# Kernel optimization log

Hardware: AMD Instinct MI355X
Metric: run time of the kernel (lower is better)

Reference implementation:

```python
import jax, jax.numpy as jnp
import numpy as np

WEIGHT = 1.0  # config['weight']


def setup_inputs() -> dict:
    key = jax.random.key(0)
    ks = jax.random.split(key, 10)
    B, N, S, C, D, E, H, V = 8, 4096, 512, 16, 1024, 256, 1024, 100000
    return {
        "span_vecs": jax.random.normal(ks[0], (B, N, D), jnp.float32),
        "ent_table": jax.random.normal(ks[1], (V, E), jnp.float32) * 0.02,
        "W1": jax.random.normal(ks[2], (D + E, H), jnp.float32) * (1.0 / np.sqrt(D + E)),
        "b1": jnp.zeros((H,), jnp.float32),
        "W2": jax.random.normal(ks[3], (H,), jnp.float32) * (1.0 / np.sqrt(H)),
        "b2": jnp.zeros((), jnp.float32),
        "targets_all": jax.random.uniform(ks[4], (B, N, C), jnp.float32),
        "linker_indices": jax.random.randint(ks[5], (B, S), 0, N, jnp.int32),
        "candidates_all": jax.random.randint(ks[6], (B, N, C), 0, V, jnp.int32),
        "candidate_lengths_all": jax.random.randint(ks[7], (B, N), 0, C + 1, jnp.int32),
    }


def reference(span_vecs, ent_table, W1, b1, W2, b2, targets_all,
              linker_indices, candidates_all, candidate_lengths_all):
    D = span_vecs.shape[-1]
    C = candidates_all.shape[-1]
    idx = linker_indices  # [B, S]

    # batched_index_select gathers over the span axis
    candidates = jnp.take_along_axis(candidates_all, idx[:, :, None], axis=1)        # [B,S,C] int
    lengths = jnp.take_along_axis(candidate_lengths_all, idx, axis=1)                # [B,S] int
    targets = jnp.take_along_axis(targets_all, idx[:, :, None], axis=1)              # [B,S,C]
    linker_vecs = jnp.take_along_axis(span_vecs, idx[:, :, None], axis=1)            # [B,S,D]

    cand_vecs = ent_table[candidates]                                                # [B,S,C,E]

    # layers: Linear(D+E,H) -> ReLU -> (dropout=identity in eval) -> Linear(H,1)
    # fused: split W1 so the [B,S,C,D+E] expanded concat is never materialized
    W1s, W1e = W1[:D], W1[D:]
    h_span = jnp.einsum('bsd,dh->bsh', linker_vecs, W1s)                             # [B,S,H]
    h_cand = jnp.einsum('bsce,eh->bsch', cand_vecs, W1e)                             # [B,S,C,H]
    h = jax.nn.relu(h_span[:, :, None, :] + h_cand + b1)
    scores = jnp.einsum('bsch,h->bsc', h, W2) + b2                                   # [B,S,C]

    # create_candidate_mask
    mask = (jnp.arange(C)[None, None, :] < lengths[:, :, None]).astype(scores.dtype)

    # BCEWithLogitsLoss(reduction='none'), masked sum * weight
    bce = jnp.maximum(scores, 0.0) - scores * targets + jnp.log1p(jnp.exp(-jnp.abs(scores)))
    loss = (mask * bce).sum() * WEIGHT

    predictions = jnp.argmax(scores - (1.0 - mask) * 1e23, axis=-1)                  # [B,S]
    return loss, scores, predictions
```

## Files before the change

### kernel.cpp

```cpp
#include <hip/hip_runtime.h>
#include <math.h>


typedef short short8 __attribute__((ext_vector_type(8)));
typedef _Float16 half8v __attribute__((ext_vector_type(8)));
typedef float f32x16 __attribute__((ext_vector_type(16)));

static __device__ inline unsigned short f2bf(float x) {
  unsigned u = __float_as_uint(x);
  unsigned r = (u + 0x7FFFu + ((u >> 16) & 1u)) >> 16;
  return (unsigned short)r;
}
static __device__ inline float bf2f(unsigned short b) {
  return __uint_as_float(((unsigned)b) << 16);
}
static __device__ inline unsigned short f2h(float x) {
  _Float16 h = (_Float16)x;
  return *(unsigned short*)&h;
}

#define GLD_TO_LDS(gp, lp)                                          \
  __builtin_amdgcn_global_load_lds(                                 \
      (const __attribute__((address_space(1))) void*)(gp),          \
      (__attribute__((address_space(3))) void*)(lp), 16, 0, 0)

static __device__ inline void split_write(unsigned short* buf, int g,
                                          float4 c0, float4 c1) {
  float xs[8] = {c0.x, c0.y, c0.z, c0.w, c1.x, c1.y, c1.z, c1.w};
  short8 h8, l8;
#pragma unroll
  for (int j = 0; j < 8; ++j) {
    unsigned short h = f2bf(xs[j]);
    h8[j] = (short)h;
    l8[j] = (short)f2bf(xs[j] - bf2f(h));
  }
  *(short8*)(buf + (g << 3)) = h8;
  *(short8*)(buf + 4096 + (g << 3)) = l8;
}

static __device__ inline void h16_write(unsigned short* buf, int g,
                                        float4 c0, float4 c1) {
  short8 v;
  v[0] = (short)f2h(c0.x); v[1] = (short)f2h(c0.y);
  v[2] = (short)f2h(c0.z); v[3] = (short)f2h(c0.w);
  v[4] = (short)f2h(c1.x); v[5] = (short)f2h(c1.y);
  v[6] = (short)f2h(c1.z); v[7] = (short)f2h(c1.w);
  *(short8*)(buf + (g << 3)) = v;
}

__global__ __launch_bounds__(256) void k_w1t(const float* __restrict__ W1,
                                             unsigned short* __restrict__ sThi,
                                             unsigned short* __restrict__ sTlo,
                                             unsigned short* __restrict__ eT16) {
  __shared__ float t[32][33];
  int n0 = blockIdx.x * 32, k0 = blockIdx.y * 32;
  int rr = threadIdx.x >> 5, cc = threadIdx.x & 31;
#pragma unroll
  for (int i = 0; i < 4; ++i)
    t[rr + 8 * i][cc] = W1[(size_t)(k0 + rr + 8 * i) * 1024 + n0 + cc];
  __syncthreads();
#pragma unroll
  for (int i = 0; i < 4; ++i) {
    int nl = rr + 8 * i;
    float v = t[cc][nl];
    int n = n0 + nl, k = k0 + cc;
    if (k0 < 1024) {
      unsigned short h = f2bf(v);
      unsigned short l = f2bf(v - bf2f(h));
      sThi[(size_t)n * 1024 + k] = h;
      sTlo[(size_t)n * 1024 + k] = l;
    } else {
      eT16[(size_t)n * 256 + (k - 1024)] = f2h(v);
    }
  }
}

template <int KSTEPS>
__global__ __launch_bounds__(256, 2) void k_g32g(
    const float* __restrict__ span, const int* __restrict__ linker,
    const unsigned short* __restrict__ Bhi, const unsigned short* __restrict__ Blo,
    float* __restrict__ Out) {
  const int tid = threadIdx.x;
  const int l = tid & 63;
  const int w = tid >> 6;
  const int wm = w >> 1, wn = w & 1;
  const int id = blockIdx.x;
  const int z = id >> 8;
  const int sid = id & 255;
  const int m8 = sid & 7;
  const int cb = (sid >> 3) & 7;
  const int q = sid >> 6;
  const int row0 = ((q << 3) + m8) << 7;
  const int col0 = cb << 7;
  const int koff = z * (KSTEPS * 32);
  Out += (size_t)z * 4194304;

  __shared__ unsigned short lds[32768];

  f32x16 acc[2][2];
#pragma unroll
  for (int i = 0; i < 2; ++i)
#pragma unroll
    for (int j = 0; j < 2; ++j)
#pragma unroll
      for (int k = 0; k < 16; ++k) acc[i][j][k] = 0.f;

  const int ar0 = tid >> 2, ap0 = tid & 3;
  const int al0c = ap0 ^ ((ar0 >> 1) & 3);
  const int ar1 = ar0 + 64;
  const int al1c = ap0 ^ ((ar1 >> 1) & 3);
  const int r0g = row0 + ar0, r1g = row0 + ar1;
  const float* asrc0 =
      span + (((size_t)(r0g >> 9) << 12) + linker[r0g]) * 1024 + koff + al0c * 8;
  const float* asrc1 =
      span + (((size_t)(r1g >> 9) << 12) + linker[r1g]) * 1024 + koff + al1c * 8;
  const size_t boff0 = (size_t)(col0 + ar0) * 1024 + al0c * 8 + koff;
  const size_t boff1 = (size_t)(col0 + ar1) * 1024 + al1c * 8 + koff;
  const int w512 = w * 512;

  {
    float4 a00 = *(const float4*)(asrc0);
    float4 a01 = *(const float4*)(asrc0 + 4);
    float4 a10 = *(const float4*)(asrc1);
    float4 a11 = *(const float4*)(asrc1 + 4);
    GLD_TO_LDS(Bhi + boff0, lds + 8192 + w512);
    GLD_TO_LDS(Bhi + boff1, lds + 10240 + w512);
    GLD_TO_LDS(Blo + boff0, lds + 12288 + w512);
    GLD_TO_LDS(Blo + boff1, lds + 14336 + w512);
    split_write(lds, tid, a00, a01);
    split_write(lds, tid + 256, a10, a11);
  }
  asm volatile("s_waitcnt vmcnt(0) lgkmcnt(0)" ::: "memory");
  __builtin_amdgcn_s_barrier();
  asm volatile("" ::: "memory");

  for (int ks = 0; ks < KSTEPS; ++ks) {
    float4 a00, a01, a10, a11;
    const int k0n = (ks + 1) * 32;
    unsigned short* bn = lds + (((ks + 1) & 1) << 14);
    if (ks + 1 < KSTEPS) {
      a00 = *(const float4*)(asrc0 + k0n);
      a01 = *(const float4*)(asrc0 + k0n + 4);
      a10 = *(const float4*)(asrc1 + k0n);
      a11 = *(const float4*)(asrc1 + k0n + 4);
      GLD_TO_LDS(Bhi + boff0 + k0n, bn + 8192 + w512);
      GLD_TO_LDS(Bhi + boff1 + k0n, bn + 10240 + w512);
      GLD_TO_LDS(Blo + boff0 + k0n, bn + 12288 + w512);
      GLD_TO_LDS(Blo + boff1 + k0n, bn + 14336 + w512);
    }

    const unsigned short* cbuf = lds + ((ks & 1) << 14);
#pragma unroll
    for (int kc = 0; kc < 2; ++kc) {
      const int kg = kc * 2 + (l >> 5);
      short8 ah[2], alv[2], bh[2], bl[2];
#pragma unroll
      for (int it = 0; it < 2; ++it) {
        int r = wm * 64 + it * 32 + (l & 31);
        int off = r * 32 + ((kg ^ ((r >> 1) & 3)) << 3);
        ah[it] = *(const short8*)(cbuf + off);
        alv[it] = *(const short8*)(cbuf + 4096 + off);
      }
#pragma unroll
      for (int jt = 0; jt < 2; ++jt) {
        int r = wn * 64 + jt * 32 + (l & 31);
        int off = r * 32 + ((kg ^ ((r >> 1) & 3)) << 3);
        bh[jt] = *(const short8*)(cbuf + 8192 + off);
        bl[jt] = *(const short8*)(cbuf + 12288 + off);
      }
#pragma unroll
      for (int it = 0; it < 2; ++it)
#pragma unroll
        for (int jt = 0; jt < 2; ++jt) {
          acc[it][jt] = __builtin_amdgcn_mfma_f32_32x32x16_bf16(
              ah[it], bh[jt], acc[it][jt], 0, 0, 0);
          acc[it][jt] = __builtin_amdgcn_mfma_f32_32x32x16_bf16(
              ah[it], bl[jt], acc[it][jt], 0, 0, 0);
          acc[it][jt] = __builtin_amdgcn_mfma_f32_32x32x16_bf16(
              alv[it], bh[jt], acc[it][jt], 0, 0, 0);
        }
    }

    if (ks + 1 < KSTEPS) {
      split_write(bn, tid, a00, a01);
      split_write(bn, tid + 256, a10, a11);
      asm volatile("s_waitcnt vmcnt(0) lgkmcnt(0)" ::: "memory");
      __builtin_amdgcn_s_barrier();
      asm volatile("" ::: "memory");
    }
  }

#pragma unroll
  for (int it = 0; it < 2; ++it) {
    int mb = row0 + wm * 64 + it * 32 + 4 * (l >> 5);
#pragma unroll
    for (int jt = 0; jt < 2; ++jt) {
      int n = col0 + wn * 64 + jt * 32 + (l & 31);
#pragma unroll
      for (int rg = 0; rg < 16; ++rg) {
        int m = mb + (rg & 3) + 8 * (rg >> 2);
        Out[(size_t)m * 1024 + n] = acc[it][jt][rg];
      }
    }
  }
}

__global__ __launch_bounds__(256, 4) void k_gf16g(
    const float* __restrict__ ent, const int* __restrict__ linker,
    const int* __restrict__ cand_all, const unsigned short* __restrict__ Bt,
    const float* __restrict__ HsIn, const float* __restrict__ b1,
    const float* __restrict__ W2, float* __restrict__ Out) {
  const int tid = threadIdx.x;
  const int l = tid & 63;
  const int w = tid >> 6;
  const int wm = w >> 1, wn = w & 1;
  const int id = blockIdx.x;
  const int m8 = id & 7;
  const int cb = (id >> 3) & 7;
  const int q = id >> 6;
  const int row0 = ((q << 3) + m8) << 7;
  const int col0 = cb << 7;

  __shared__ unsigned short lds[16384];

  f32x16 acc[2][2];
#pragma unroll
  for (int i = 0; i < 2; ++i)
#pragma unroll
    for (int j = 0; j < 2; ++j)
#pragma unroll
      for (int k = 0; k < 16; ++k) acc[i][j][k] = 0.f;

  const int ar0 = tid >> 2, ap0 = tid & 3;
  const int al0c = ap0 ^ ((ar0 >> 1) & 3);
  const int ar1 = ar0 + 64;
  const int al1c = ap0 ^ ((ar1 >> 1) & 3);
  const int s0 = row0 + ar0, s1 = row0 + ar1;
  const int cid0 =
      cand_all[(((size_t)(s0 >> 13) << 12) + linker[s0 >> 4]) * 16 + (s0 & 15)];
  const int cid1 =
      cand_all[(((size_t)(s1 >> 13) << 12) + linker[s1 >> 4]) * 16 + (s1 & 15)];
  const float* asrc0 = ent + ((size_t)cid0 << 8) + al0c * 8;
  const float* asrc1 = ent + ((size_t)cid1 << 8) + al1c * 8;
  const size_t boff0 = (size_t)(col0 + ar0) * 256 + al0c * 8;
  const size_t boff1 = (size_t)(col0 + ar1) * 256 + al1c * 8;
  const int w512 = w * 512;

  {
    float4 a00 = *(const float4*)(asrc0);
    float4 a01 = *(const float4*)(asrc0 + 4);
    float4 a10 = *(const float4*)(asrc1);
    float4 a11 = *(const float4*)(asrc1 + 4);
    GLD_TO_LDS(Bt + boff0, lds + 4096 + w512);
    GLD_TO_LDS(Bt + boff1, lds + 6144 + w512);
    h16_write(lds, tid, a00, a01);
    h16_write(lds, tid + 256, a10, a11);
  }
  asm volatile("s_waitcnt vmcnt(0) lgkmcnt(0)" ::: "memory");
  __builtin_amdgcn_s_barrier();
  asm volatile("" ::: "memory");

#pragma unroll 2
  for (int ks = 0; ks < 8; ++ks) {
    float4 a00, a01, a10, a11;
    const int k0n = (ks + 1) * 32;
    unsigned short* bn = lds + (((ks + 1) & 1) << 13);
    if (ks + 1 < 8) {
      a00 = *(const float4*)(asrc0 + k0n);
      a01 = *(const float4*)(asrc0 + k0n + 4);
      a10 = *(const float4*)(asrc1 + k0n);
      a11 = *(const float4*)(asrc1 + k0n + 4);
      GLD_TO_LDS(Bt + boff0 + k0n, bn + 4096 + w512);
      GLD_TO_LDS(Bt + boff1 + k0n, bn + 6144 + w512);
    }

    const unsigned short* cbuf = lds + ((ks & 1) << 13);
#pragma unroll
    for (int kc = 0; kc < 2; ++kc) {
      const int kg = kc * 2 + (l >> 5);
      half8v av[2], bv[2];
#pragma unroll
      for (int it = 0; it < 2; ++it) {
        int r = wm * 64 + it * 32 + (l & 31);
        int off = r * 32 + ((kg ^ ((r >> 1) & 3)) << 3);
        av[it] = *(const half8v*)(cbuf + off);
      }
#pragma unroll
      for (int jt = 0; jt < 2; ++jt) {
        int r = wn * 64 + jt * 32 + (l & 31);
        int off = r * 32 + ((kg ^ ((r >> 1) & 3)) << 3);
        bv[jt] = *(const half8v*)(cbuf + 4096 + off);
      }
#pragma unroll
      for (int it = 0; it < 2; ++it)
#pragma unroll
        for (int jt = 0; jt < 2; ++jt)
          acc[it][jt] = __builtin_amdgcn_mfma_f32_32x32x16_f16(
              av[it], bv[jt], acc[it][jt], 0, 0, 0);
    }

    if (ks + 1 < 8) {
      h16_write(bn, tid, a00, a01);
      h16_write(bn, tid + 256, a10, a11);
      asm volatile("s_waitcnt vmcnt(0) lgkmcnt(0)" ::: "memory");
      __builtin_amdgcn_s_barrier();
      asm volatile("" ::: "memory");
    }
  }

  float sv[2][16];
#pragma unroll
  for (int it = 0; it < 2; ++it) {
#pragma unroll
    for (int rg = 0; rg < 16; ++rg) sv[it][rg] = 0.f;
    const int p0 = (row0 + wm * 64 + it * 32) >> 4;
#pragma unroll
    for (int jt = 0; jt < 2; ++jt) {
      int n = col0 + wn * 64 + jt * 32 + (l & 31);
      float b1v = b1[n], w2v = W2[n];
      float add0 = HsIn[(size_t)p0 * 1024 + n] +
                   HsIn[4194304 + (size_t)p0 * 1024 + n] + b1v;
      float add1 = HsIn[(size_t)(p0 + 1) * 1024 + n] +
                   HsIn[4194304 + (size_t)(p0 + 1) * 1024 + n] + b1v;
#pragma unroll
      for (int rg = 0; rg < 16; ++rg) {
        float h = fmaxf(acc[it][jt][rg] + (rg < 8 ? add0 : add1), 0.f);
        sv[it][rg] = fmaf(h, w2v, sv[it][rg]);
      }
    }
  }
  __syncthreads();
  float* scf = (float*)lds;
  const int cc0 = l & 31, lh4 = 4 * (l >> 5);
#pragma unroll
  for (int it = 0; it < 2; ++it)
#pragma unroll
    for (int rg = 0; rg < 16; ++rg) {
      int row = (rg & 3) + 8 * (rg >> 2) + lh4;
      scf[((w * 2 + it) * 32 + row) * 32 + ((cc0 + row) & 31)] = sv[it][rg];
    }
  __syncthreads();
  int gr = tid >> 1, h = tid & 1;
  int r = gr & 31, itv = (gr >> 5) & 1, wmv = gr >> 6;
  const float* sa = scf + ((wmv * 4 + itv) * 32 + r) * 32;
  const float* sb = scf + ((wmv * 4 + 2 + itv) * 32 + r) * 32;
  float sum = 0.f;
#pragma unroll
  for (int j = 0; j < 16; ++j) {
    int cidx = (h * 16 + j + r) & 31;
    sum += sa[cidx] + sb[cidx];
  }
  sum += __shfl_xor(sum, 1, 64);
  if (h == 0) Out[(size_t)cb * 65536 + row0 + gr] = sum;
}

__global__ __launch_bounds__(64) void k_final8(const float* __restrict__ score8,
                                               const float* __restrict__ b2p,
                                               const float* __restrict__ targets_all,
                                               const int* __restrict__ linker,
                                               const int* __restrict__ len_all,
                                               float* __restrict__ out) {
  int p = blockIdx.x * 64 + threadIdx.x;
  float b2 = b2p[0];
  int b = p >> 9;
  int i = linker[p];
  int len = len_all[(b << 12) + i];
  const float* tg = targets_all + ((((size_t)b << 12) + (size_t)i) << 4);

  float sc[16];
#pragma unroll
  for (int c = 0; c < 16; ++c) sc[c] = b2;
#pragma unroll
  for (int c8 = 0; c8 < 8; ++c8) {
    const float4* q4 = (const float4*)(score8 + (size_t)c8 * 65536 + p * 16);
#pragma unroll
    for (int j = 0; j < 4; ++j) {
      float4 v = q4[j];
      sc[j * 4 + 0] += v.x; sc[j * 4 + 1] += v.y;
      sc[j * 4 + 2] += v.z; sc[j * 4 + 3] += v.w;
    }
  }

  float loss = 0.f;
  float best = -INFINITY;
  int bc = 0;
#pragma unroll
  for (int c = 0; c < 16; ++c) {
    float s = sc[c];
    out[1 + p * 16 + c] = s;
    float val;
    if (c < len) {
      float t = tg[c];
      loss += fmaxf(s, 0.f) - s * t + log1pf(expf(-fabsf(s)));
      val = s;
    } else {
      val = s - 1e23f;
    }
    if (val > best) { best = val; bc = c; }
  }
  out[1 + 65536 + p] = (float)bc;

  for (int off = 32; off > 0; off >>= 1) loss += __shfl_down(loss, off, 64);
  if (threadIdx.x == 0) atomicAdd(out, loss);
}

#define BM 128
#define BN 128
#define BK 16
#define PAD 4

__global__ __launch_bounds__(256) void k_prep(const int* __restrict__ linker,
                                              const int* __restrict__ cand_all,
                                              int* __restrict__ cand_ids) {
  int g = blockIdx.x * 256 + threadIdx.x;
  int pair = g >> 4;
  int c = g & 15;
  int b = pair >> 9;
  int i = linker[pair];
  cand_ids[g] = cand_all[(((size_t)b << 12) + (size_t)i) * 16 + c];
}

__global__ __launch_bounds__(256) void k_hs(const float* __restrict__ span,
                                            const float* __restrict__ W1,
                                            const int* __restrict__ linker,
                                            float* __restrict__ Hs) {
  const int tid = threadIdx.x;
  const int tx = tid & 15, ty = tid >> 4;
  const int row0 = blockIdx.y * BM;
  const int col0 = blockIdx.x * BN;
  __shared__ float As[BK][BM + PAD];
  __shared__ float Bs[BK][BN + PAD];
  __shared__ int rows_g[BM];
  if (tid < BM) {
    int m = row0 + tid;
    int b = m >> 9;
    rows_g[tid] = (b << 12) + linker[m];
  }
  __syncthreads();
  float acc[8][8] = {};
  for (int k0 = 0; k0 < 1024; k0 += BK) {
#pragma unroll
    for (int ll = 0; ll < 2; ++ll) {
      int f = tid + ll * 256;
      int r = f >> 2;
      int kk = (f & 3) << 2;
      const float4 v = *(const float4*)(span + (size_t)rows_g[r] * 1024 + k0 + kk);
      As[kk + 0][r] = v.x; As[kk + 1][r] = v.y;
      As[kk + 2][r] = v.z; As[kk + 3][r] = v.w;
    }
#pragma unroll
    for (int ll = 0; ll < 2; ++ll) {
      int f = tid + ll * 256;
      int kk = f >> 5;
      int nn = (f & 31) << 2;
      *(float4*)&Bs[kk][nn] = *(const float4*)(W1 + (size_t)(k0 + kk) * 1024 + col0 + nn);
    }
    __syncthreads();
#pragma unroll
    for (int k = 0; k < BK; ++k) {
      float a[8], b[8];
      *(float4*)&a[0] = *(const float4*)&As[k][ty * 8];
      *(float4*)&a[4] = *(const float4*)&As[k][ty * 8 + 4];
      *(float4*)&b[0] = *(const float4*)&Bs[k][tx * 8];
      *(float4*)&b[4] = *(const float4*)&Bs[k][tx * 8 + 4];
#pragma unroll
      for (int i = 0; i < 8; ++i)
#pragma unroll
        for (int j = 0; j < 8; ++j) acc[i][j] = fmaf(a[i], b[j], acc[i][j]);
    }
    __syncthreads();
  }
#pragma unroll
  for (int i = 0; i < 8; ++i) {
    int m = row0 + ty * 8 + i;
    float* dst = Hs + (size_t)m * 1024 + col0 + tx * 8;
    *(float4*)dst = *(float4*)&acc[i][0];
    *(float4*)(dst + 4) = *(float4*)&acc[i][4];
  }
}

__global__ __launch_bounds__(256) void k_hc(const float* __restrict__ ent,
                                            const float* __restrict__ W1,
                                            const int* __restrict__ cand_ids,
                                            const float* __restrict__ Hs,
                                            const float* __restrict__ b1,
                                            const float* __restrict__ W2,
                                            float* __restrict__ score_ws) {
  const int tid = threadIdx.x;
  const int tx = tid & 15, ty = tid >> 4;
  const int row0 = blockIdx.y * BM;
  const int col0 = blockIdx.x * BN;
  __shared__ float As[BK][BM + PAD];
  __shared__ float Bs[BK][BN + PAD];
  __shared__ int rows_g[BM];
  __shared__ float red[BM][17];
  if (tid < BM) rows_g[tid] = cand_ids[row0 + tid];
  __syncthreads();
  float acc[8][8] = {};
  for (int k0 = 0; k0 < 256; k0 += BK) {
#pragma unroll
    for (int ll = 0; ll < 2; ++ll) {
      int f = tid + ll * 256;
      int r = f >> 2;
      int kk = (f & 3) << 2;
      const float4 v = *(const float4*)(ent + (size_t)rows_g[r] * 256 + k0 + kk);
      As[kk + 0][r] = v.x; As[kk + 1][r] = v.y;
      As[kk + 2][r] = v.z; As[kk + 3][r] = v.w;
    }
#pragma unroll
    for (int ll = 0; ll < 2; ++ll) {
      int f = tid + ll * 256;
      int kk = f >> 5;
      int nn = (f & 31) << 2;
      *(float4*)&Bs[kk][nn] =
          *(const float4*)(W1 + (size_t)(1024 + k0 + kk) * 1024 + col0 + nn);
    }
    __syncthreads();
#pragma unroll
    for (int k = 0; k < BK; ++k) {
      float a[8], b[8];
      *(float4*)&a[0] = *(const float4*)&As[k][ty * 8];
      *(float4*)&a[4] = *(const float4*)&As[k][ty * 8 + 4];
      *(float4*)&b[0] = *(const float4*)&Bs[k][tx * 8];
      *(float4*)&b[4] = *(const float4*)&Bs[k][tx * 8 + 4];
#pragma unroll
      for (int i = 0; i < 8; ++i)
#pragma unroll
        for (int j = 0; j < 8; ++j) acc[i][j] = fmaf(a[i], b[j], acc[i][j]);
    }
    __syncthreads();
  }
  const int pair = (row0 + ty * 8) >> 4;
  float hsv[8], b1v[8], w2v[8];
  {
    const float* hp = Hs + (size_t)pair * 1024 + col0 + tx * 8;
    *(float4*)&hsv[0] = *(const float4*)hp;
    *(float4*)&hsv[4] = *(const float4*)(hp + 4);
    const float* bp = b1 + col0 + tx * 8;
    *(float4*)&b1v[0] = *(const float4*)bp;
    *(float4*)&b1v[4] = *(const float4*)(bp + 4);
    const float* wp = W2 + col0 + tx * 8;
    *(float4*)&w2v[0] = *(const float4*)wp;
    *(float4*)&w2v[4] = *(const float4*)(wp + 4);
  }
#pragma unroll
  for (int i = 0; i < 8; ++i) {
    float s = 0.f;
#pragma unroll
    for (int j = 0; j < 8; ++j) {
      float h = acc[i][j] + hsv[j] + b1v[j];
      h = fmaxf(h, 0.f);
      s = fmaf(h, w2v[j], s);
    }
    red[ty * 8 + i][tx] = s;
  }
  __syncthreads();
  if (tid < BM) {
    float s = 0.f;
#pragma unroll
    for (int x = 0; x < 16; ++x) s += red[tid][x];
    atomicAdd(&score_ws[row0 + tid], s);
  }
}

__global__ __launch_bounds__(256) void k_final(const float* __restrict__ score_ws,
                                               const float* __restrict__ b2p,
                                               const float* __restrict__ targets_all,
                                               const int* __restrict__ linker,
                                               const int* __restrict__ len_all,
                                               float* __restrict__ out) {
  int p = blockIdx.x * 256 + threadIdx.x;
  float b2 = b2p[0];
  int b = p >> 9;
  int i = linker[p];
  int len = len_all[(b << 12) + i];
  const float* tg = targets_all + ((((size_t)b << 12) + (size_t)i) << 4);

  float loss = 0.f;
  float best = -INFINITY;
  int bc = 0;
#pragma unroll
  for (int c = 0; c < 16; ++c) {
    float sc = score_ws[p * 16 + c] + b2;
    out[1 + p * 16 + c] = sc;
    float val;
    if (c < len) {
      float t = tg[c];
      loss += fmaxf(sc, 0.f) - sc * t + log1pf(expf(-fabsf(sc)));
      val = sc;
    } else {
      val = sc - 1e23f;
    }
    if (val > best) { best = val; bc = c; }
  }
  out[1 + 65536 + p] = (float)bc;

  for (int off = 32; off > 0; off >>= 1) loss += __shfl_down(loss, off, 64);
  if ((threadIdx.x & 63) == 0) atomicAdd(out, loss);
}

extern "C" void kernel_launch(void* const* d_in, const int* in_sizes, int n_in,
                              void* d_out, int out_size, void* d_ws,
                              size_t ws_size, hipStream_t stream) {
  const float* span    = (const float*)d_in[0];
  const float* ent     = (const float*)d_in[1];
  const float* W1      = (const float*)d_in[2];
  const float* b1      = (const float*)d_in[3];
  const float* W2      = (const float*)d_in[4];
  const float* b2      = (const float*)d_in[5];
  const float* targets = (const float*)d_in[6];
  const int* linker    = (const int*)d_in[7];
  const int* cand_all  = (const int*)d_in[8];
  const int* len_all   = (const int*)d_in[9];
  float* out = (float*)d_out;

  char* ws = (char*)d_ws;
  float* Hs       = (float*)(ws + 0);
  float* score8   = (float*)(ws + 33554432);
  unsigned short* sTh  = (unsigned short*)(ws + 35651584);
  unsigned short* sTl  = (unsigned short*)(ws + 37748736);
  unsigned short* eT16 = (unsigned short*)(ws + 39845888);
  float* score_ws = (float*)(ws + 40370176);
  int* cand_ids   = (int*)(ws + 40632320);
  const size_t NEED_MFMA = 40894464;

  hipMemsetAsync(d_out, 0, sizeof(float), stream);

  if (ws_size >= NEED_MFMA) {
    k_w1t<<<dim3(32, 40), dim3(256), 0, stream>>>(W1, sTh, sTl, eT16);
    k_g32g<16><<<dim3(512), dim3(256), 0, stream>>>(span, linker, sTh, sTl, Hs);
    k_gf16g<<<dim3(4096), dim3(256), 0, stream>>>(ent, linker, cand_all, eT16,
                                                  Hs, b1, W2, score8);
    k_final8<<<dim3(64), dim3(64), 0, stream>>>(score8, b2, targets, linker,
                                                len_all, out);
  } else {
    hipMemsetAsync(score_ws, 0, 65536 * sizeof(float), stream);
    k_prep<<<dim3(256), dim3(256), 0, stream>>>(linker, cand_all, cand_ids);
    dim3 g1(8, 32);
    k_hs<<<g1, dim3(256), 0, stream>>>(span, W1, linker, Hs);
    dim3 g2(8, 512);
    k_hc<<<g2, dim3(256), 0, stream>>>(ent, W1, cand_ids, Hs, b1, W2, score_ws);
    k_final<<<dim3(16), dim3(256), 0, stream>>>(score_ws, b2, targets, linker,
                                                len_all, out);
  }
}
```

Measured before the change: 339.3 us.

## Pre-gather candidate embeddings to fp16 buffer and stream via direct LDS loads

Adds a prep phase, merged into the W1 transpose kernel, that gathers the candidate entity rows, converts them to fp16 and writes them into a contiguous workspace buffer. The main candidate GEMM then loads A tiles with global_load_lds like B, dropping the per-iteration fp32 register loads and conversions. The cost is an extra 32MB fp16 write and read-back pass and a larger workspace requirement, traded for a simpler, better pipelined GEMM inner loop.

```diff
diff --git a/kernel.cpp b/kernel.cpp
--- a/kernel.cpp
+++ b/kernel.cpp
@@ -38,39 +38,44 @@
   *(short8*)(buf + 4096 + (g << 3)) = l8;
 }
 
-static __device__ inline void h16_write(unsigned short* buf, int g,
-                                        float4 c0, float4 c1) {
-  short8 v;
-  v[0] = (short)f2h(c0.x); v[1] = (short)f2h(c0.y);
-  v[2] = (short)f2h(c0.z); v[3] = (short)f2h(c0.w);
-  v[4] = (short)f2h(c1.x); v[5] = (short)f2h(c1.y);
-  v[6] = (short)f2h(c1.z); v[7] = (short)f2h(c1.w);
-  *(short8*)(buf + (g << 3)) = v;
-}
-
-__global__ __launch_bounds__(256) void k_w1t(const float* __restrict__ W1,
-                                             unsigned short* __restrict__ sThi,
-                                             unsigned short* __restrict__ sTlo,
-                                             unsigned short* __restrict__ eT16) {
+__global__ __launch_bounds__(256) void k_prep_e(
+    const float* __restrict__ ent, const float* __restrict__ W1,
+    const int* __restrict__ linker, const int* __restrict__ cand_all,
+    unsigned short* __restrict__ A2, unsigned short* __restrict__ sThi,
+    unsigned short* __restrict__ sTlo, unsigned short* __restrict__ eT16) {
   __shared__ float t[32][33];
-  int n0 = blockIdx.x * 32, k0 = blockIdx.y * 32;
-  int rr = threadIdx.x >> 5, cc = threadIdx.x & 31;
-#pragma unroll
-  for (int i = 0; i < 4; ++i)
-    t[rr + 8 * i][cc] = W1[(size_t)(k0 + rr + 8 * i) * 1024 + n0 + cc];
-  __syncthreads();
-#pragma unroll
-  for (int i = 0; i < 4; ++i) {
-    int nl = rr + 8 * i;
-    float v = t[cc][nl];
-    int n = n0 + nl, k = k0 + cc;
-    if (k0 < 1024) {
-      unsigned short h = f2bf(v);
-      unsigned short l = f2bf(v - bf2f(h));
-      sThi[(size_t)n * 1024 + k] = h;
-      sTlo[(size_t)n * 1024 + k] = l;
-    } else {
-      eT16[(size_t)n * 256 + (k - 1024)] = f2h(v);
+  const int bx = blockIdx.x;
+  if (bx < 16384) {
+    int f = bx * 256 + threadIdx.x;
+    int row = f >> 6;
+    int pair = row >> 4;
+    int b = pair >> 9;
+    int i = linker[pair];
+    int cid = cand_all[(((size_t)b << 12) + (size_t)i) * 16 + (row & 15)];
+    const float4 v = *((const float4*)(ent + ((size_t)cid << 8)) + (f & 63));
+    *(ushort4*)(A2 + ((size_t)f << 2)) =
+        make_ushort4(f2h(v.x), f2h(v.y), f2h(v.z), f2h(v.w));
+  } else {
+    int b2x = bx - 16384;
+    int n0 = (b2x & 31) * 32, k0 = (b2x >> 5) * 32;
+    int rr = threadIdx.x >> 5, cc = threadIdx.x & 31;
+#pragma unroll
+    for (int i = 0; i < 4; ++i)
+      t[rr + 8 * i][cc] = W1[(size_t)(k0 + rr + 8 * i) * 1024 + n0 + cc];
+    __syncthreads();
+#pragma unroll
+    for (int i = 0; i < 4; ++i) {
+      int nl = rr + 8 * i;
+      float v = t[cc][nl];
+      int n = n0 + nl, k = k0 + cc;
+      if (k0 < 1024) {
+        unsigned short h = f2bf(v);
+        unsigned short l = f2bf(v - bf2f(h));
+        sThi[(size_t)n * 1024 + k] = h;
+        sTlo[(size_t)n * 1024 + k] = l;
+      } else {
+        eT16[(size_t)n * 256 + (k - 1024)] = f2h(v);
+      }
     }
   }
 }
@@ -205,9 +210,9 @@
   }
 }
 
-__global__ __launch_bounds__(256, 4) void k_gf16g(
-    const float* __restrict__ ent, const int* __restrict__ linker,
-    const int* __restrict__ cand_all, const unsigned short* __restrict__ Bt,
+__global__ __launch_bounds__(256, 4) void k_gf16(
+    const unsigned short* __restrict__ A,
+    const unsigned short* __restrict__ Bt,
     const float* __restrict__ HsIn, const float* __restrict__ b1,
     const float* __restrict__ W2, float* __restrict__ Out) {
   const int tid = threadIdx.x;
@@ -233,45 +238,31 @@
 
   const int ar0 = tid >> 2, ap0 = tid & 3;
   const int al0c = ap0 ^ ((ar0 >> 1) & 3);
-  const int ar1 = ar0 + 64;
+  const int ar1 = (tid + 256) >> 2;
   const int al1c = ap0 ^ ((ar1 >> 1) & 3);
-  const int s0 = row0 + ar0, s1 = row0 + ar1;
-  const int cid0 =
-      cand_all[(((size_t)(s0 >> 13) << 12) + linker[s0 >> 4]) * 16 + (s0 & 15)];
-  const int cid1 =
-      cand_all[(((size_t)(s1 >> 13) << 12) + linker[s1 >> 4]) * 16 + (s1 & 15)];
-  const float* asrc0 = ent + ((size_t)cid0 << 8) + al0c * 8;
-  const float* asrc1 = ent + ((size_t)cid1 << 8) + al1c * 8;
+  const size_t aoff0 = (size_t)(row0 + ar0) * 256 + al0c * 8;
+  const size_t aoff1 = (size_t)(row0 + ar1) * 256 + al1c * 8;
   const size_t boff0 = (size_t)(col0 + ar0) * 256 + al0c * 8;
   const size_t boff1 = (size_t)(col0 + ar1) * 256 + al1c * 8;
   const int w512 = w * 512;
 
-  {
-    float4 a00 = *(const float4*)(asrc0);
-    float4 a01 = *(const float4*)(asrc0 + 4);
-    float4 a10 = *(const float4*)(asrc1);
-    float4 a11 = *(const float4*)(asrc1 + 4);
-    GLD_TO_LDS(Bt + boff0, lds + 4096 + w512);
-    GLD_TO_LDS(Bt + boff1, lds + 6144 + w512);
-    h16_write(lds, tid, a00, a01);
-    h16_write(lds, tid + 256, a10, a11);
-  }
-  asm volatile("s_waitcnt vmcnt(0) lgkmcnt(0)" ::: "memory");
+  GLD_TO_LDS(A + aoff0, lds + w512);
+  GLD_TO_LDS(A + aoff1, lds + 2048 + w512);
+  GLD_TO_LDS(Bt + boff0, lds + 4096 + w512);
+  GLD_TO_LDS(Bt + boff1, lds + 6144 + w512);
+  asm volatile("s_waitcnt vmcnt(0)" ::: "memory");
   __builtin_amdgcn_s_barrier();
   asm volatile("" ::: "memory");
 
 #pragma unroll 2
   for (int ks = 0; ks < 8; ++ks) {
-    float4 a00, a01, a10, a11;
-    const int k0n = (ks + 1) * 32;
-    unsigned short* bn = lds + (((ks + 1) & 1) << 13);
     if (ks + 1 < 8) {
-      a00 = *(const float4*)(asrc0 + k0n);
-      a01 = *(const float4*)(asrc0 + k0n + 4);
-      a10 = *(const float4*)(asrc1 + k0n);
-      a11 = *(const float4*)(asrc1 + k0n + 4);
-      GLD_TO_LDS(Bt + boff0 + k0n, bn + 4096 + w512);
-      GLD_TO_LDS(Bt + boff1 + k0n, bn + 6144 + w512);
+      const int k0 = (ks + 1) * 32;
+      unsigned short* b = lds + (((ks + 1) & 1) << 13);
+      GLD_TO_LDS(A + aoff0 + k0, b + w512);
+      GLD_TO_LDS(A + aoff1 + k0, b + 2048 + w512);
+      GLD_TO_LDS(Bt + boff0 + k0, b + 4096 + w512);
+      GLD_TO_LDS(Bt + boff1 + k0, b + 6144 + w512);
     }
 
     const unsigned short* cbuf = lds + ((ks & 1) << 13);
@@ -300,9 +291,7 @@
     }
 
     if (ks + 1 < 8) {
-      h16_write(bn, tid, a00, a01);
-      h16_write(bn, tid + 256, a10, a11);
-      asm volatile("s_waitcnt vmcnt(0) lgkmcnt(0)" ::: "memory");
+      asm volatile("s_waitcnt vmcnt(0)" ::: "memory");
       __builtin_amdgcn_s_barrier();
       asm volatile("" ::: "memory");
     }
@@ -617,20 +606,21 @@
   char* ws = (char*)d_ws;
   float* Hs       = (float*)(ws + 0);
   float* score8   = (float*)(ws + 33554432);
-  unsigned short* sTh  = (unsigned short*)(ws + 35651584);
-  unsigned short* sTl  = (unsigned short*)(ws + 37748736);
-  unsigned short* eT16 = (unsigned short*)(ws + 39845888);
-  float* score_ws = (float*)(ws + 40370176);
-  int* cand_ids   = (int*)(ws + 40632320);
-  const size_t NEED_MFMA = 40894464;
+  unsigned short* A2   = (unsigned short*)(ws + 35651584);
+  unsigned short* sTh  = (unsigned short*)(ws + 69206016);
+  unsigned short* sTl  = (unsigned short*)(ws + 71303168);
+  unsigned short* eT16 = (unsigned short*)(ws + 73400320);
+  float* score_ws = (float*)(ws + 73924608);
+  int* cand_ids   = (int*)(ws + 74186752);
+  const size_t NEED_MFMA = 74448896;
 
   hipMemsetAsync(d_out, 0, sizeof(float), stream);
 
   if (ws_size >= NEED_MFMA) {
-    k_w1t<<<dim3(32, 40), dim3(256), 0, stream>>>(W1, sTh, sTl, eT16);
+    k_prep_e<<<dim3(17664), dim3(256), 0, stream>>>(
+        ent, W1, linker, cand_all, A2, sTh, sTl, eT16);
     k_g32g<16><<<dim3(512), dim3(256), 0, stream>>>(span, linker, sTh, sTl, Hs);
-    k_gf16g<<<dim3(4096), dim3(256), 0, stream>>>(ent, linker, cand_all, eT16,
-                                                  Hs, b1, W2, score8);
+    k_gf16<<<dim3(4096), dim3(256), 0, stream>>>(A2, eT16, Hs, b1, W2, score8);
     k_final8<<<dim3(64), dim3(64), 0, stream>>>(score8, b2, targets, linker,
                                                 len_all, out);
   } else {
```

New measurement: 342.8 us. Within noise of the previous version (+1.0%).
